# Kernel optimization log

Measured on AMD Instinct MI355X. Metric: run time of the kernel, lower is better.

## Reference

```python
import jax, jax.numpy as jnp
import numpy as np

VOCAB, EMBED, HIDDEN, NUM_CELLS = 32000, 256, 512, 2
B, T = 16, 256


def setup_inputs() -> dict:
    key = jax.random.key(0)
    ks = jax.random.split(key, 10)
    s = 0.02
    return {
        "x": jax.random.randint(ks[0], (B, T), 0, VOCAB),
        "assignments": jax.random.randint(ks[1], (VOCAB,), 0, NUM_CELLS),
        "init_h": jnp.zeros((B, HIDDEN), jnp.float32),
        "init_c": jnp.zeros((B, HIDDEN), jnp.float32),
        "embed_table": jax.random.normal(ks[2], (VOCAB, EMBED), jnp.float32) * s,
        "W_ih": jax.random.normal(ks[3], (NUM_CELLS, 4 * HIDDEN, EMBED), jnp.float32) * s,
        "W_hh": jax.random.normal(ks[4], (NUM_CELLS, 4 * HIDDEN, HIDDEN), jnp.float32) * s,
        "b": jax.random.normal(ks[5], (NUM_CELLS, 4 * HIDDEN), jnp.float32) * s,  # b_ih + b_hh combined
        "W_out": jax.random.normal(ks[6], (VOCAB, HIDDEN), jnp.float32) * s,
        "b_out": jnp.zeros((VOCAB,), jnp.float32),
    }


def reference(x, assignments, init_h, init_c, embed_table, W_ih, W_hh, b, W_out, b_out):
    # embedding lookup (dropout is identity in eval mode)
    emb = embed_table[x]              # [B, T, E]
    cell_ids = assignments[x]         # [B, T] -> which LSTMCell weight set per token

    def step(carry, inp):
        h, c = carry
        x_t, cid = inp                # x_t [B,E], cid [B]
        # gates for every cell's weights, then per-element select by assigned cell
        gates = (jnp.einsum('be,cge->cbg', x_t, W_ih)
                 + jnp.einsum('bh,cgh->cbg', h, W_hh)
                 + b[:, None, :])     # [C, B, 4H]
        g_sel = jnp.take_along_axis(gates, cid[None, :, None], axis=0)[0]  # [B,4H]
        i, f, g, o = jnp.split(g_sel, 4, axis=-1)  # torch LSTMCell gate order i,f,g,o
        c2 = jax.nn.sigmoid(f) * c + jax.nn.sigmoid(i) * jnp.tanh(g)
        h2 = jax.nn.sigmoid(o) * jnp.tanh(c2)
        return (h2, c2), h2

    (hT, cT), hs = jax.lax.scan(step, (init_h, init_c),
                                (jnp.transpose(emb, (1, 0, 2)), cell_ids.T))
    out = jnp.transpose(hs, (1, 0, 2)).reshape(-1, HIDDEN)  # [B*T, H]
    logits = jax.nn.log_softmax(out @ W_out.T + b_out, axis=-1)  # [B*T, V]
    return logits, hT, cT
```

## Files before the change

kernel.cpp:

```cpp
#include <hip/hip_runtime.h>

#define T_STEPS 256
#define BATCH   16
#define EMBED   256
#define HIDDEN  512
#define G4      2048
#define VOCAB   32000
#define NTOK    4096
#define NBLK_SCAN 64

typedef _Float16 f16x8 __attribute__((ext_vector_type(8)));
typedef float    f32x4 __attribute__((ext_vector_type(4)));

#define OFF_GIN    0
#define OFF_WOUT   33554432
#define OFF_HS     66322432
#define OFF_EMB    70516736
#define OFF_WIH    72613888
#define OFF_HPUB   74711040
#define OFF_CIDT   74743808
#define OFF_CIDR   74760192
#define OFF_FLAGS  74776576

#define P_SA 4096000
#define P_SB (P_SA + 262144)
#define P_SC (P_SB + 262144)
#define P_SD (P_SC + 4096)
#define P_SE (P_SD + 257)

__global__ __launch_bounds__(256) void prep_kernel(
    const int* __restrict__ x, const int* __restrict__ assign,
    const float* __restrict__ Wih, const float* __restrict__ Wout,
    const float* __restrict__ embt,
    _Float16* __restrict__ wih_h, _Float16* __restrict__ wout_h,
    _Float16* __restrict__ emb_h, int* __restrict__ cids_t,
    int* __restrict__ cid_r, unsigned int* __restrict__ flags)
{
    size_t id = (size_t)blockIdx.x * 256 + threadIdx.x;
    if (id < P_SA) {
        float4 v = ((const float4*)Wout)[id];
        _Float16* o = wout_h + id * 4;
        o[0] = (_Float16)v.x; o[1] = (_Float16)v.y; o[2] = (_Float16)v.z; o[3] = (_Float16)v.w;
    } else if (id < P_SB) {
        size_t j = id - P_SA;
        float4 v = ((const float4*)Wih)[j];
        _Float16* o = wih_h + j * 4;
        o[0] = (_Float16)v.x; o[1] = (_Float16)v.y; o[2] = (_Float16)v.z; o[3] = (_Float16)v.w;
    } else if (id < P_SC) {
        size_t j = id - P_SB;
        int r  = (int)(j >> 6);
        int e4 = (int)(j & 63);
        float4 v = ((const float4*)(embt + (size_t)x[r] * EMBED))[e4];
        _Float16* o = emb_h + (size_t)r * EMBED + e4 * 4;
        o[0] = (_Float16)v.x; o[1] = (_Float16)v.y; o[2] = (_Float16)v.z; o[3] = (_Float16)v.w;
    } else if (id < P_SD) {
        int j = (int)(id - P_SC);
        int b = j >> 8, t = j & 255;
        int c = assign[x[j]];
        cid_r[j] = c;
        cids_t[t * BATCH + b] = c;
    } else if (id < P_SE) {
        flags[id - P_SD] = 0u;
    }
}

__global__ __launch_bounds__(256) void gin_gemm_kernel(
    const _Float16* __restrict__ A,
    const _Float16* __restrict__ WihH,
    const float* __restrict__ bias,
    const int* __restrict__ cid_r,
    float* __restrict__ Gin)
{
    __shared__ __attribute__((aligned(16))) _Float16 As[128][32];
    __shared__ __attribute__((aligned(16))) _Float16 Bs[128][32];
    const int tid = threadIdx.x, lane = tid & 63, w = tid >> 6;
    const int m16 = lane & 15, kq = lane >> 4;
    const int rb = blockIdx.x, nb = blockIdx.y, cell = blockIdx.z;
    const _Float16* Bt = WihH + (size_t)cell * G4 * EMBED;
    f32x4 acc[2][8];
    for (int mt = 0; mt < 2; mt++) for (int nt = 0; nt < 8; nt++) acc[mt][nt] = (f32x4){0.f,0.f,0.f,0.f};

    for (int kt = 0; kt < EMBED; kt += 32) {
        __syncthreads();
        #pragma unroll
        for (int c = tid; c < 512; c += 256) {
            int row = c >> 2, q = c & 3;
            ((uint4*)As)[c] = ((const uint4*)(A  + (size_t)(rb*128 + row) * EMBED + kt))[q];
            ((uint4*)Bs)[c] = ((const uint4*)(Bt + (size_t)(nb*128 + row) * EMBED + kt))[q];
        }
        __syncthreads();
        f16x8 af[2], bf[8];
        #pragma unroll
        for (int mt = 0; mt < 2; mt++) af[mt] = *(const f16x8*)&As[w*32 + mt*16 + m16][kq*8];
        #pragma unroll
        for (int nt = 0; nt < 8; nt++) bf[nt] = *(const f16x8*)&Bs[nt*16 + m16][kq*8];
        #pragma unroll
        for (int mt = 0; mt < 2; mt++)
            #pragma unroll
            for (int nt = 0; nt < 8; nt++)
                acc[mt][nt] = __builtin_amdgcn_mfma_f32_16x16x32_f16(af[mt], bf[nt], acc[mt][nt], 0, 0, 0);
    }
    #pragma unroll
    for (int mt = 0; mt < 2; mt++)
        #pragma unroll
        for (int nt = 0; nt < 8; nt++) {
            int grow = nb*128 + nt*16 + m16;
            float bo = bias[cell * G4 + grow];
            #pragma unroll
            for (int i = 0; i < 4; i++) {
                int r = rb*128 + w*32 + mt*16 + kq*4 + i;
                if (cid_r[r] == cell) {
                    int bb = r >> 8, tt = r & 255;
                    Gin[((size_t)tt * G4 + grow) * BATCH + bb] = acc[mt][nt][i] + bo;
                }
            }
        }
}

__device__ __forceinline__ float sigf(float x)   { return 1.f / (1.f + __expf(-x)); }
__device__ __forceinline__ float tanh_s(float x) { float e = __expf(2.f * x); return 1.f - 2.f / (e + 1.f); }

#define SCAN_LDS_BYTES (65536 + 4352 + 4096)

__global__ __launch_bounds__(256) void scan_kernel(
    const float* __restrict__ Whh,
    const float* __restrict__ init_h,
    const float* __restrict__ init_c,
    const float* __restrict__ Gin,
    const int* __restrict__ cids_t,
    _Float16* __restrict__ h_pub,
    _Float16* __restrict__ hs,
    unsigned int* __restrict__ flags,
    float* __restrict__ outHT, float* __restrict__ outCT)
{
    extern __shared__ char smem[];
    _Float16*      hs_lds   = (_Float16*)smem;
    float*         gate_lds = (float*)(smem + 65536);
    unsigned char* cid_lds  = (unsigned char*)(smem + 65536 + 4352);

    const int tid = threadIdx.x, lane = tid & 63, w = tid >> 6;
    const int blk = blockIdx.x;
    const int cell = w >> 1, mt = w & 1;
    const int m16 = lane & 15, kq = lane >> 4;

    int r    = mt * 16 + m16;
    int g    = r >> 3, ul = r & 7;
    int grow = g * HIDDEN + blk * 8 + ul;
    f16x8 af[16];
    const float* wrow = Whh + ((size_t)cell * G4 + grow) * HIDDEN;
    #pragma unroll
    for (int kt = 0; kt < 16; kt++) {
        int k0 = kt * 32 + kq * 8;
        float4 a0 = *(const float4*)(wrow + k0);
        float4 a1 = *(const float4*)(wrow + k0 + 4);
        f16x8 f;
        f[0]=(_Float16)a0.x; f[1]=(_Float16)a0.y; f[2]=(_Float16)a0.z; f[3]=(_Float16)a0.w;
        f[4]=(_Float16)a1.x; f[5]=(_Float16)a1.y; f[6]=(_Float16)a1.z; f[7]=(_Float16)a1.w;
        af[kt] = f;
    }

    for (int i = tid; i < T_STEPS * BATCH; i += 256)
        cid_lds[i] = (unsigned char)cids_t[i];

    const int ub = tid >> 3, uu = tid & 7;
    const int ug = blk * 8 + uu;
    float c_st = 0.f;
    if (tid < 128) {
        c_st = init_c[ub * HIDDEN + ug];
        float h0 = init_h[ub * HIDDEN + ug];
        h_pub[ub * HIDDEN + ug] = (_Float16)h0;
    }
    __syncthreads();
    if (tid == 0) {
        __builtin_amdgcn_fence(__ATOMIC_RELEASE, "agent");
        __hip_atomic_store(&flags[blk], 1u, __ATOMIC_RELAXED, __HIP_MEMORY_SCOPE_AGENT);
    }

    for (int t = 0; t < T_STEPS; t++) {
        float pf0, pf1, pf2, pf3;
        if (tid < 128) {
            const float* gbase = Gin + (size_t)t * (G4 * BATCH);
            pf0 = gbase[((size_t)0 * HIDDEN + ug) * BATCH + ub];
            pf1 = gbase[((size_t)1 * HIDDEN + ug) * BATCH + ub];
            pf2 = gbase[((size_t)2 * HIDDEN + ug) * BATCH + ub];
            pf3 = gbase[((size_t)3 * HIDDEN + ug) * BATCH + ub];
        }

        if (w == 0) {
            const unsigned tgt = (unsigned)(t + 1);
            while (__hip_atomic_load(&flags[lane], __ATOMIC_ACQUIRE, __HIP_MEMORY_SCOPE_AGENT) < tgt) {}
        }
        __syncthreads();

        const _Float16* hb = h_pub + (size_t)(t & 1) * (BATCH * HIDDEN);
        f32x4 acc = (f32x4){0.f, 0.f, 0.f, 0.f};
        #pragma unroll
        for (int kt = 0; kt < 16; kt++) {
            int k0 = kt * 32 + kq * 8;
            f16x8 bfrag = *(const f16x8*)(hb + m16 * HIDDEN + k0);
            acc = __builtin_amdgcn_mfma_f32_16x16x32_f16(af[kt], bfrag, acc, 0, 0, 0);
        }
        #pragma unroll
        for (int i = 0; i < 4; i++) {
            int rr = mt * 16 + kq * 4 + i;
            gate_lds[(cell * 32 + rr) * 17 + m16] = acc[i];
        }
        __syncthreads();

        if (tid < 128) {
            int cid = cid_lds[t * BATCH + ub];
            float gi = gate_lds[(cid * 32 +  0 + uu) * 17 + ub] + pf0;
            float gf = gate_lds[(cid * 32 +  8 + uu) * 17 + ub] + pf1;
            float gg = gate_lds[(cid * 32 + 16 + uu) * 17 + ub] + pf2;
            float go = gate_lds[(cid * 32 + 24 + uu) * 17 + ub] + pf3;
            float is = sigf(gi), fs = sigf(gf), os = sigf(go);
            c_st = fs * c_st + is * tanh_s(gg);
            float hn = os * tanh_s(c_st);
            _Float16 hh = (_Float16)hn;
            h_pub[(size_t)((t + 1) & 1) * (BATCH * HIDDEN) + ub * HIDDEN + ug] = hh;
            hs_lds[t * 128 + tid] = hh;
            if (t == T_STEPS - 1) {
                outHT[ub * HIDDEN + ug] = hn;
                outCT[ub * HIDDEN + ug] = c_st;
            }
        }
        __syncthreads();
        if (tid == 0) {
            __builtin_amdgcn_fence(__ATOMIC_RELEASE, "agent");
            __hip_atomic_store(&flags[blk], (unsigned)(t + 2), __ATOMIC_RELAXED, __HIP_MEMORY_SCOPE_AGENT);
        }
    }

    __syncthreads();
    for (int id = tid; id < T_STEPS * BATCH; id += 256) {
        int t = id >> 4, b = id & 15;
        uint4 v = *(const uint4*)(hs_lds + t * 128 + b * 8);
        *(uint4*)(hs + ((size_t)b * T_STEPS + t) * HIDDEN + blk * 8) = v;
    }
}

__global__ __launch_bounds__(256) void gemm_out_kernel(
    const _Float16* __restrict__ A,
    const _Float16* __restrict__ Bt,
    const float* __restrict__ bout,
    float* __restrict__ C)
{
    __shared__ __attribute__((aligned(16))) _Float16 As[128][32];
    __shared__ __attribute__((aligned(16))) _Float16 Bs[128][32];
    const int tid = threadIdx.x, lane = tid & 63, w = tid >> 6;
    const int m16 = lane & 15, kq = lane >> 4;
    const int rb = blockIdx.x, nb = blockIdx.y;
    f32x4 acc[2][8];
    for (int mt = 0; mt < 2; mt++) for (int nt = 0; nt < 8; nt++) acc[mt][nt] = (f32x4){0.f,0.f,0.f,0.f};

    for (int kt = 0; kt < HIDDEN; kt += 32) {
        __syncthreads();
        #pragma unroll
        for (int c = tid; c < 512; c += 256) {
            int row = c >> 2, q = c & 3;
            ((uint4*)As)[c] = ((const uint4*)(A  + (size_t)(rb*128 + row) * HIDDEN + kt))[q];
            ((uint4*)Bs)[c] = ((const uint4*)(Bt + (size_t)(nb*128 + row) * HIDDEN + kt))[q];
        }
        __syncthreads();
        f16x8 af[2], bf[8];
        #pragma unroll
        for (int mt = 0; mt < 2; mt++) af[mt] = *(const f16x8*)&As[w*32 + mt*16 + m16][kq*8];
        #pragma unroll
        for (int nt = 0; nt < 8; nt++) bf[nt] = *(const f16x8*)&Bs[nt*16 + m16][kq*8];
        #pragma unroll
        for (int mt = 0; mt < 2; mt++)
            #pragma unroll
            for (int nt = 0; nt < 8; nt++)
                acc[mt][nt] = __builtin_amdgcn_mfma_f32_16x16x32_f16(af[mt], bf[nt], acc[mt][nt], 0, 0, 0);
    }
    #pragma unroll
    for (int mt = 0; mt < 2; mt++)
        #pragma unroll
        for (int nt = 0; nt < 8; nt++) {
            int vcol = nb*128 + nt*16 + m16;
            float bo = bout[vcol];
            #pragma unroll
            for (int i = 0; i < 4; i++) {
                int r = rb*128 + w*32 + mt*16 + kq*4 + i;
                C[(size_t)r * VOCAB + vcol] = acc[mt][nt][i] + bo;
            }
        }
}

__global__ __launch_bounds__(1024) void lsm_kernel(float* __restrict__ C)
{
    extern __shared__ float sm[];
    float* red = sm + VOCAB;
    const int tid = threadIdx.x, lane = tid & 63, wid = tid >> 6;
    float* rowp = C + (size_t)blockIdx.x * VOCAB;
    const float4* src4 = (const float4*)rowp;
    float4* dst4 = (float4*)rowp;
    float4* row4 = (float4*)sm;

    float m = -3.0e38f;
    for (int i = tid; i < VOCAB/4; i += 1024) {
        float4 v = src4[i];
        row4[i] = v;
        m = fmaxf(m, fmaxf(fmaxf(v.x, v.y), fmaxf(v.z, v.w)));
    }
    #pragma unroll
    for (int o = 32; o; o >>= 1) m = fmaxf(m, __shfl_xor(m, o));
    if (lane == 0) red[wid] = m;
    __syncthreads();
    if (tid == 0) {
        float mm = red[0];
        for (int i = 1; i < 16; i++) mm = fmaxf(mm, red[i]);
        red[16] = mm;
    }
    __syncthreads();
    m = red[16];

    float s = 0.f;
    for (int i = tid; i < VOCAB/4; i += 1024) {
        float4 v = row4[i];
        s += __expf(v.x - m) + __expf(v.y - m) + __expf(v.z - m) + __expf(v.w - m);
    }
    #pragma unroll
    for (int o = 32; o; o >>= 1) s += __shfl_xor(s, o);
    if (lane == 0) red[wid + 32] = s;
    __syncthreads();
    if (tid == 0) {
        float ss = 0.f;
        for (int i = 0; i < 16; i++) ss += red[32 + i];
        red[17] = ss;
    }
    __syncthreads();
    const float lse = m + __logf(red[17]);

    for (int i = tid; i < VOCAB/4; i += 1024) {
        float4 v = row4[i];
        v.x -= lse; v.y -= lse; v.z -= lse; v.w -= lse;
        dst4[i] = v;
    }
}

extern "C" void kernel_launch(void* const* d_in, const int* in_sizes, int n_in,
                              void* d_out, int out_size, void* d_ws, size_t ws_size,
                              hipStream_t stream) {
    (void)in_sizes; (void)n_in; (void)out_size; (void)ws_size;
    const int*   x      = (const int*)d_in[0];
    const int*   assign = (const int*)d_in[1];
    const float* init_h = (const float*)d_in[2];
    const float* init_c = (const float*)d_in[3];
    const float* embt   = (const float*)d_in[4];
    const float* Wih    = (const float*)d_in[5];
    const float* Whh    = (const float*)d_in[6];
    const float* bias   = (const float*)d_in[7];
    const float* Wout   = (const float*)d_in[8];
    const float* bout   = (const float*)d_in[9];
    float* out = (float*)d_out;
    char*  ws  = (char*)d_ws;

    float*        Gin    = (float*)(ws + OFF_GIN);
    _Float16*     wout_h = (_Float16*)(ws + OFF_WOUT);
    _Float16*     hs     = (_Float16*)(ws + OFF_HS);
    _Float16*     emb_h  = (_Float16*)(ws + OFF_EMB);
    _Float16*     wih_h  = (_Float16*)(ws + OFF_WIH);
    _Float16*     h_pub  = (_Float16*)(ws + OFF_HPUB);
    int*          cids_t = (int*)(ws + OFF_CIDT);
    int*          cid_r  = (int*)(ws + OFF_CIDR);
    unsigned int* flags  = (unsigned int*)(ws + OFF_FLAGS);

    float* outHT = out + (size_t)NTOK * VOCAB;
    float* outCT = outHT + BATCH * HIDDEN;

    prep_kernel<<<(P_SE + 255) / 256, 256, 0, stream>>>(
        x, assign, Wih, Wout, embt, wih_h, wout_h, emb_h, cids_t, cid_r, flags);

    gin_gemm_kernel<<<dim3(NTOK/128, G4/128, 2), 256, 0, stream>>>(
        emb_h, wih_h, bias, cid_r, Gin);

    hipFuncSetAttribute((const void*)scan_kernel,
                        hipFuncAttributeMaxDynamicSharedMemorySize, SCAN_LDS_BYTES);
    scan_kernel<<<NBLK_SCAN, 256, SCAN_LDS_BYTES, stream>>>(
        Whh, init_h, init_c, Gin, cids_t, h_pub, hs, flags, outHT, outCT);

    gemm_out_kernel<<<dim3(NTOK/128, VOCAB/128), 256, 0, stream>>>(
        hs, wout_h, bout, out);

    static_assert(VOCAB % 4 == 0, "");
    int lsm_lds = (VOCAB + 64) * (int)sizeof(float);
    hipFuncSetAttribute((const void*)lsm_kernel,
                        hipFuncAttributeMaxDynamicSharedMemorySize, lsm_lds);
    lsm_kernel<<<NTOK, 1024, lsm_lds, stream>>>(out);
}
```

Before: 2.708 ms.

## Replace flag-based grid barrier with per-word step-tagged hidden-state exchange

The scan kernel no longer publishes h to a buffer and then waits on per-block flags. Each 64-bit word now carries two fp16 hidden values plus a step tag, and consumers spin on the tags of exactly the words they need, loading them straight into MFMA B fragments. This removes the release fence, the flag polling and two __syncthreads per step, aiming to cut per-step cross-block latency. The exchange buffer lives in the output logits region, which gemm_out later overwrites. The cost is 64 relaxed atomic loads per lane with possible respins, and higher register pressure.

```diff
diff --git a/kernel.cpp b/kernel.cpp
--- a/kernel.cpp
+++ b/kernel.cpp
@@ -11,6 +11,7 @@
 
 typedef _Float16 f16x8 __attribute__((ext_vector_type(8)));
 typedef float    f32x4 __attribute__((ext_vector_type(4)));
+typedef unsigned long long u64;
 
 #define OFF_GIN    0
 #define OFF_WOUT   33554432
@@ -20,21 +21,20 @@
 #define OFF_HPUB   74711040
 #define OFF_CIDT   74743808
 #define OFF_CIDR   74760192
-#define OFF_FLAGS  74776576
 
 #define P_SA 4096000
 #define P_SB (P_SA + 262144)
 #define P_SC (P_SB + 262144)
 #define P_SD (P_SC + 4096)
-#define P_SE (P_SD + 257)
+#define P_SE (P_SD + 8192)
 
 __global__ __launch_bounds__(256) void prep_kernel(
     const int* __restrict__ x, const int* __restrict__ assign,
     const float* __restrict__ Wih, const float* __restrict__ Wout,
-    const float* __restrict__ embt,
+    const float* __restrict__ embt, const float* __restrict__ init_h,
     _Float16* __restrict__ wih_h, _Float16* __restrict__ wout_h,
     _Float16* __restrict__ emb_h, int* __restrict__ cids_t,
-    int* __restrict__ cid_r, unsigned int* __restrict__ flags)
+    int* __restrict__ cid_r, u64* __restrict__ hch)
 {
     size_t id = (size_t)blockIdx.x * 256 + threadIdx.x;
     if (id < P_SA) {
@@ -60,7 +60,19 @@
         cid_r[j] = c;
         cids_t[t * BATCH + b] = c;
     } else if (id < P_SE) {
-        flags[id - P_SD] = 0u;
+        int j = (int)(id - P_SD);
+        int buf = j >> 12, r = j & 4095;
+        int sb = r >> 6, b = (r >> 2) & 15, jj = r & 3;
+        u64 val = 0ull;
+        if (buf == 0) {
+            int u0 = sb * 8 + jj * 2;
+            _Float16 h0 = (_Float16)init_h[b * HIDDEN + u0];
+            _Float16 h1 = (_Float16)init_h[b * HIDDEN + u0 + 1];
+            unsigned p = (unsigned)__builtin_bit_cast(unsigned short, h0)
+                       | ((unsigned)__builtin_bit_cast(unsigned short, h1) << 16);
+            val = (u64)p | (1ull << 32);
+        }
+        __hip_atomic_store(hch + j, val, __ATOMIC_RELAXED, __HIP_MEMORY_SCOPE_AGENT);
     }
 }
 
@@ -124,13 +136,11 @@
 
 __global__ __launch_bounds__(256) void scan_kernel(
     const float* __restrict__ Whh,
-    const float* __restrict__ init_h,
     const float* __restrict__ init_c,
     const float* __restrict__ Gin,
     const int* __restrict__ cids_t,
-    _Float16* __restrict__ h_pub,
+    u64* __restrict__ hch,
     _Float16* __restrict__ hs,
-    unsigned int* __restrict__ flags,
     float* __restrict__ outHT, float* __restrict__ outCT)
 {
     extern __shared__ char smem[];
@@ -165,16 +175,10 @@
     const int ub = tid >> 3, uu = tid & 7;
     const int ug = blk * 8 + uu;
     float c_st = 0.f;
-    if (tid < 128) {
-        c_st = init_c[ub * HIDDEN + ug];
-        float h0 = init_h[ub * HIDDEN + ug];
-        h_pub[ub * HIDDEN + ug] = (_Float16)h0;
-    }
-    __syncthreads();
-    if (tid == 0) {
-        __builtin_amdgcn_fence(__ATOMIC_RELEASE, "agent");
-        __hip_atomic_store(&flags[blk], 1u, __ATOMIC_RELAXED, __HIP_MEMORY_SCOPE_AGENT);
-    }
+    if (tid < 128) c_st = init_c[ub * HIDDEN + ug];
+    __syncthreads();
+
+    const int laneoff = kq * 64 + m16 * 4;
 
     for (int t = 0; t < T_STEPS; t++) {
         float pf0, pf1, pf2, pf3;
@@ -186,19 +190,28 @@
             pf3 = gbase[((size_t)3 * HIDDEN + ug) * BATCH + ub];
         }
 
-        if (w == 0) {
-            const unsigned tgt = (unsigned)(t + 1);
-            while (__hip_atomic_load(&flags[lane], __ATOMIC_ACQUIRE, __HIP_MEMORY_SCOPE_AGENT) < tgt) {}
-        }
-        __syncthreads();
-
-        const _Float16* hb = h_pub + (size_t)(t & 1) * (BATCH * HIDDEN);
+        u64 ch[64];
+        u64* hb = hch + (size_t)(t & 1) * 4096 + laneoff;
+        #pragma unroll
+        for (int kt = 0; kt < 16; kt++)
+            #pragma unroll
+            for (int j = 0; j < 4; j++)
+                ch[kt * 4 + j] = __hip_atomic_load(hb + kt * 256 + j,
+                                                   __ATOMIC_RELAXED, __HIP_MEMORY_SCOPE_AGENT);
+        const unsigned want = (unsigned)(t + 1);
+        #pragma unroll
+        for (int i = 0; i < 64; i++)
+            while ((unsigned)(ch[i] >> 32) != want)
+                ch[i] = __hip_atomic_load(hb + (i >> 2) * 256 + (i & 3),
+                                          __ATOMIC_RELAXED, __HIP_MEMORY_SCOPE_AGENT);
+
         f32x4 acc = (f32x4){0.f, 0.f, 0.f, 0.f};
         #pragma unroll
         for (int kt = 0; kt < 16; kt++) {
-            int k0 = kt * 32 + kq * 8;
-            f16x8 bfrag = *(const f16x8*)(hb + m16 * HIDDEN + k0);
-            acc = __builtin_amdgcn_mfma_f32_16x16x32_f16(af[kt], bfrag, acc, 0, 0, 0);
+            union { f16x8 v; unsigned u[4]; } bb;
+            #pragma unroll
+            for (int j = 0; j < 4; j++) bb.u[j] = (unsigned)ch[kt * 4 + j];
+            acc = __builtin_amdgcn_mfma_f32_16x16x32_f16(af[kt], bb.v, acc, 0, 0, 0);
         }
         #pragma unroll
         for (int i = 0; i < 4; i++) {
@@ -217,17 +230,20 @@
             c_st = fs * c_st + is * tanh_s(gg);
             float hn = os * tanh_s(c_st);
             _Float16 hh = (_Float16)hn;
-            h_pub[(size_t)((t + 1) & 1) * (BATCH * HIDDEN) + ub * HIDDEN + ug] = hh;
+            unsigned hu = (unsigned)__builtin_bit_cast(unsigned short, hh);
+            unsigned other = (unsigned)__shfl_xor((int)hu, 1);
+            if (!(uu & 1)) {
+                unsigned packed = hu | (other << 16);
+                u64 val = (u64)packed | ((u64)(t + 2) << 32);
+                u64* dst = hch + (size_t)((t + 1) & 1) * 4096
+                               + (size_t)blk * 64 + ub * 4 + (uu >> 1);
+                __hip_atomic_store(dst, val, __ATOMIC_RELAXED, __HIP_MEMORY_SCOPE_AGENT);
+            }
             hs_lds[t * 128 + tid] = hh;
             if (t == T_STEPS - 1) {
                 outHT[ub * HIDDEN + ug] = hn;
                 outCT[ub * HIDDEN + ug] = c_st;
             }
-        }
-        __syncthreads();
-        if (tid == 0) {
-            __builtin_amdgcn_fence(__ATOMIC_RELEASE, "agent");
-            __hip_atomic_store(&flags[blk], (unsigned)(t + 2), __ATOMIC_RELAXED, __HIP_MEMORY_SCOPE_AGENT);
         }
     }
 
@@ -361,16 +377,16 @@
     _Float16*     hs     = (_Float16*)(ws + OFF_HS);
     _Float16*     emb_h  = (_Float16*)(ws + OFF_EMB);
     _Float16*     wih_h  = (_Float16*)(ws + OFF_WIH);
-    _Float16*     h_pub  = (_Float16*)(ws + OFF_HPUB);
     int*          cids_t = (int*)(ws + OFF_CIDT);
     int*          cid_r  = (int*)(ws + OFF_CIDR);
-    unsigned int* flags  = (unsigned int*)(ws + OFF_FLAGS);
+
+    u64* hch = (u64*)out;
 
     float* outHT = out + (size_t)NTOK * VOCAB;
     float* outCT = outHT + BATCH * HIDDEN;
 
     prep_kernel<<<(P_SE + 255) / 256, 256, 0, stream>>>(
-        x, assign, Wih, Wout, embt, wih_h, wout_h, emb_h, cids_t, cid_r, flags);
+        x, assign, Wih, Wout, embt, init_h, wih_h, wout_h, emb_h, cids_t, cid_r, hch);
 
     gin_gemm_kernel<<<dim3(NTOK/128, G4/128, 2), 256, 0, stream>>>(
         emb_h, wih_h, bias, cid_r, Gin);
@@ -378,7 +394,7 @@
     hipFuncSetAttribute((const void*)scan_kernel,
                         hipFuncAttributeMaxDynamicSharedMemorySize, SCAN_LDS_BYTES);
     scan_kernel<<<NBLK_SCAN, 256, SCAN_LDS_BYTES, stream>>>(
-        Whh, init_h, init_c, Gin, cids_t, h_pub, hs, flags, outHT, outCT);
+        Whh, init_c, Gin, cids_t, hch, hs, outHT, outCT);
 
     gemm_out_kernel<<<dim3(NTOK/128, VOCAB/128), 256, 0, stream>>>(
         hs, wout_h, bout, out);
```

Result: slower. 3.931 ms (+45.2%).
